# Optimization experiments

Hardware: AMD Instinct MI355X
Metric: run time of the kernel (lower is better)

## Reference

```python
import jax, jax.numpy as jnp
import numpy as np

DIM, HEADS, DIM_HEAD = 256, 8, 32  # dim == heads * dim_head
EPS = 1e-5


def setup_inputs() -> dict:
    key = jax.random.key(0)
    ks = jax.random.split(key, 6)
    B, C, H, W = 16, DIM, 64, 64
    x = jax.random.normal(ks[0], (B, C, H, W), dtype=jnp.float32)
    # 1x1 conv weights stored as [out_ch, in_ch]
    w_qkv = jax.random.normal(ks[1], (3 * DIM, DIM), dtype=jnp.float32) * (1.0 / np.sqrt(DIM))
    w_out = jax.random.normal(ks[2], (DIM, DIM), dtype=jnp.float32) * (1.0 / np.sqrt(DIM))
    b_out = jax.random.normal(ks[3], (DIM,), dtype=jnp.float32) * 0.01
    ln_gamma = jnp.ones((DIM,), dtype=jnp.float32)
    ln_beta = jnp.zeros((DIM,), dtype=jnp.float32)
    return {"x": x, "w_qkv": w_qkv, "w_out": w_out, "b_out": b_out,
            "ln_gamma": ln_gamma, "ln_beta": ln_beta}


def _linear_attention(x, w_qkv, w_out, b_out, ln_gamma, ln_beta):
    B, C, H, W = x.shape
    d = C // HEADS
    # 1x1 conv == channel matmul
    qkv = jnp.einsum('bchw,oc->bohw', x, w_qkv)  # [B, 3C, H, W]
    q, k, v = jnp.split(qkv, 3, axis=1)
    # 'b (h d) x y -> b h x y d'
    def split_heads(t):
        t = t.reshape(B, HEADS, d, H, W)
        return t.transpose(0, 1, 3, 4, 2)  # b h x y d
    q, k, v = split_heads(q), split_heads(k), split_heads(v)
    q = jax.nn.softmax(q, axis=-1)   # over d (channel) dim
    k = jax.nn.softmax(k, axis=-2)   # over y spatial axis (faithful to torch dim=-2)
    context = jnp.einsum('bhxyd,bhxye->bhde', k, v)          # [B,H,d,d]
    out = jnp.einsum('bhde,bhxye->bhxyd', context, q)        # [B,H,X,Y,d]
    # 'b h x y d -> b (h d) x y'
    out = out.transpose(0, 1, 4, 2, 3).reshape(B, C, H, W)
    # output 1x1 conv + bias
    out = jnp.einsum('bchw,oc->bohw', out, w_out) + b_out[None, :, None, None]
    # LayerNorm over channel dim (permute to NHWC, norm last axis, permute back)
    y = out.transpose(0, 2, 3, 1)  # b h w c
    mu = jnp.mean(y, axis=-1, keepdims=True)
    var = jnp.var(y, axis=-1, keepdims=True)
    y = (y - mu) / jnp.sqrt(var + EPS) * ln_gamma + ln_beta
    return y.transpose(0, 3, 1, 2)


def reference(x, w_qkv, w_out, b_out, ln_gamma, ln_beta):
    return _linear_attention(x, w_qkv, w_out, b_out, ln_gamma, ln_beta)
```

## Files before the change

kernel.cpp:

```cpp
#include <hip/hip_runtime.h>
#include <hip/hip_bf16.h>

#define NB 16
#define CDIM 256
#define NHEADS 8
#define DH 32
#define NSP 4096
#define O3 768

typedef __bf16 bf16;
typedef bf16 bf16x4 __attribute__((ext_vector_type(4)));
typedef bf16 bf16x8 __attribute__((ext_vector_type(8)));
typedef float f32x4 __attribute__((ext_vector_type(4)));
typedef float f32x16 __attribute__((ext_vector_type(16)));

static __device__ __forceinline__ float bf2f(bf16 x){ return (float)x; }
static __device__ __forceinline__ bf16 f2bf(float x){ return (bf16)x; }

static __device__ __forceinline__ void gld16(const bf16* g, bf16* l){
    __builtin_amdgcn_global_load_lds((const __attribute__((address_space(1))) void*)g,
                                     (__attribute__((address_space(3))) void*)l, 16, 0, 0);
}

__global__ void k_transpose(const float* __restrict__ x, bf16* __restrict__ xT){
    __shared__ bf16 tile[64][72];
    int b = blockIdx.z;
    int c0 = blockIdx.y * 64;
    int n0 = blockIdx.x * 64;
    int t = threadIdx.x;
    const float* xb = x + (size_t)b * CDIM * NSP;
    #pragma unroll
    for (int i = 0; i < 4; ++i){
        int lin = i*256 + t;
        int c = lin >> 4;
        int n4 = (lin & 15) * 4;
        f32x4 f = *(const f32x4*)(xb + (size_t)(c0 + c)*NSP + n0 + n4);
        bf16x4 v4;
        #pragma unroll
        for (int j = 0; j < 4; ++j) v4[j] = f2bf(f[j]);
        *(bf16x4*)&tile[c][n4] = v4;
    }
    __syncthreads();
    bf16* xTb = xT + (size_t)b * NSP * CDIM;
    #pragma unroll
    for (int i = 0; i < 2; ++i){
        int lin = i*256 + t;
        int n = lin >> 3;
        int c8 = (lin & 7) * 8;
        bf16x8 v;
        #pragma unroll
        for (int j = 0; j < 8; ++j) v[j] = tile[c8+j][n];
        *(bf16x8*)(xTb + (size_t)(n0+n)*CDIM + c0 + c8) = v;
    }
}

__global__ void k_wcvt(const float* __restrict__ w, bf16* __restrict__ w2){
    int idx = (blockIdx.x*256 + threadIdx.x) * 4;
    f32x4 f = *(const f32x4*)(w + idx);
    bf16x4 v;
    #pragma unroll
    for (int j=0;j<4;j++) v[j] = f2bf(f[j]);
    *(bf16x4*)(w2 + idx) = v;
}

__global__ __launch_bounds__(512) void k_q(const bf16* __restrict__ w2,
                                           const bf16* __restrict__ xT,
                                           bf16* __restrict__ qT){
    __shared__ union {
        bf16 Bs[32768];
        bf16 ep[64*264];
    } sm;
    int bid = blockIdx.x;
    int xcd = bid & 7, slot = bid >> 3;
    int g = xcd*64 + slot;
    int b  = g >> 5;
    int n0 = (g & 31) * 128;
    int t = threadIdx.x;
    int wv = t >> 6, lane = t & 63;

    #pragma unroll
    for (int j=0;j<8;j++){
        int base_r = wv*16 + j*2;
        int r = base_r + (lane>>5);
        int c = (lane & 31) ^ (r & 7);
        gld16(xT + ((size_t)b*NSP + n0 + r)*CDIM + c*8, &sm.Bs[(size_t)base_r*256]);
    }
    __syncthreads();

    int brow[8], brx[8];
    #pragma unroll
    for (int ni=0;ni<8;ni++){
        int r = ni*16 + (lane&15);
        brow[ni] = r*32; brx[ni] = r & 7;
    }
    int arow = wv*32 + (lane&15);
    int acol = (lane>>4)*8;

    f32x4 acc[2][8];
    #pragma unroll
    for (int i=0;i<16;i++) ((f32x4*)acc)[i] = (f32x4){0.f,0.f,0.f,0.f};

    bf16x8 af0 = *(const bf16x8*)(w2 + (size_t)(arow     )*CDIM + acol);
    bf16x8 af1 = *(const bf16x8*)(w2 + (size_t)(arow + 16)*CDIM + acol);
    #pragma unroll
    for (int k0=0;k0<8;k0++){
        bf16x8 an0, an1;
        if (k0 < 7){
            an0 = *(const bf16x8*)(w2 + (size_t)(arow     )*CDIM + (k0+1)*32 + acol);
            an1 = *(const bf16x8*)(w2 + (size_t)(arow + 16)*CDIM + (k0+1)*32 + acol);
        }
        int cbase = (lane>>4) + k0*4;
        bf16x8 bfr[8];
        #pragma unroll
        for (int ni=0;ni<8;ni++)
            bfr[ni] = *(const bf16x8*)&sm.Bs[(size_t)(brow[ni] + (cbase ^ brx[ni]))*8];
        #pragma unroll
        for (int ni=0;ni<8;ni++)
            acc[0][ni] = __builtin_amdgcn_mfma_f32_16x16x32_bf16(af0, bfr[ni], acc[0][ni], 0, 0, 0);
        #pragma unroll
        for (int ni=0;ni<8;ni++)
            acc[1][ni] = __builtin_amdgcn_mfma_f32_16x16x32_bf16(af1, bfr[ni], acc[1][ni], 0, 0, 0);
        af0 = an0; af1 = an1;
    }

    #pragma unroll
    for (int ni=0;ni<8;ni++){
        float mx = -1e30f;
        #pragma unroll
        for (int mi=0;mi<2;mi++)
            #pragma unroll
            for (int r=0;r<4;r++) mx = fmaxf(mx, acc[mi][ni][r]);
        mx = fmaxf(mx, __shfl_xor(mx, 16, 64));
        mx = fmaxf(mx, __shfl_xor(mx, 32, 64));
        float s = 0.f;
        #pragma unroll
        for (int mi=0;mi<2;mi++)
            #pragma unroll
            for (int r=0;r<4;r++){
                float e = __expf(acc[mi][ni][r] - mx);
                acc[mi][ni][r] = e; s += e;
            }
        s += __shfl_xor(s, 16, 64);
        s += __shfl_xor(s, 32, 64);
        float inv = 1.f/s;
        #pragma unroll
        for (int mi=0;mi<2;mi++)
            #pragma unroll
            for (int r=0;r<4;r++) acc[mi][ni][r] *= inv;
    }

    bf16* qTb = qT + (size_t)b * NSP * CDIM;
    #pragma unroll
    for (int ph=0; ph<2; ++ph){
        __syncthreads();
        #pragma unroll
        for (int mi=0;mi<2;mi++)
            #pragma unroll
            for (int q=0;q<4;q++){
                int ni = ph*4 + q;
                int n_loc = q*16 + (lane&15);
                int o_loc = wv*32 + mi*16 + (lane>>4)*4;
                bf16x4 v4;
                #pragma unroll
                for (int r=0;r<4;r++) v4[r] = f2bf(acc[mi][ni][r]);
                *(bf16x4*)&sm.ep[n_loc*264 + o_loc] = v4;
            }
        __syncthreads();
        #pragma unroll
        for (int i=0;i<4;i++){
            int task = i*512 + t;
            int n_loc = task >> 5, seg = task & 31;
            bf16x8 v = *(const bf16x8*)&sm.ep[n_loc*264 + seg*8];
            *(bf16x8*)(qTb + (size_t)(n0 + ph*64 + n_loc)*CDIM + seg*8) = v;
        }
    }
}

__global__ __launch_bounds__(1024,4) void k_kvctx(const bf16* __restrict__ w2,
                                                  const bf16* __restrict__ xT,
                                                  float* __restrict__ ctx_p){
    __shared__ union {
        bf16 Bs[32768];
        bf16 cb[32768];
    } sm;
    int bid = blockIdx.x;
    int xcd = bid & 7, slot = bid >> 3;
    int g = xcd*64 + slot;
    int b = g >> 5;
    int ntile = g & 31;
    int n0 = ntile * 128;
    int t = threadIdx.x;
    int wv = t >> 6, lane = t & 63;

    #pragma unroll
    for (int j=0;j<4;j++){
        int base_r = wv*8 + j*2;
        int r = base_r + (lane>>5);
        int c = (lane & 31) ^ (r & 7);
        gld16(xT + ((size_t)b*NSP + n0 + r)*CDIM + c*8, &sm.Bs[(size_t)base_r*256]);
    }
    __syncthreads();

    int brow[8], brx[8];
    #pragma unroll
    for (int ni=0;ni<8;ni++){
        int r = ni*16 + (lane&15);
        brow[ni] = r*32; brx[ni] = r & 7;
    }
    int arow = 256 + wv*32 + (lane&15);
    int acol = (lane>>4)*8;

    f32x4 acc[2][8];
    #pragma unroll
    for (int i=0;i<16;i++) ((f32x4*)acc)[i] = (f32x4){0.f,0.f,0.f,0.f};

    bf16x8 af0 = *(const bf16x8*)(w2 + (size_t)(arow     )*CDIM + acol);
    bf16x8 af1 = *(const bf16x8*)(w2 + (size_t)(arow + 16)*CDIM + acol);
    #pragma unroll
    for (int k0=0;k0<8;k0++){
        bf16x8 an0, an1;
        if (k0 < 7){
            an0 = *(const bf16x8*)(w2 + (size_t)(arow     )*CDIM + (k0+1)*32 + acol);
            an1 = *(const bf16x8*)(w2 + (size_t)(arow + 16)*CDIM + (k0+1)*32 + acol);
        }
        int cbase = (lane>>4) + k0*4;
        bf16x8 bfr[8];
        #pragma unroll
        for (int ni=0;ni<8;ni++)
            bfr[ni] = *(const bf16x8*)&sm.Bs[(size_t)(brow[ni] + (cbase ^ brx[ni]))*8];
        #pragma unroll
        for (int ni=0;ni<8;ni++)
            acc[0][ni] = __builtin_amdgcn_mfma_f32_16x16x32_bf16(af0, bfr[ni], acc[0][ni], 0, 0, 0);
        #pragma unroll
        for (int ni=0;ni<8;ni++)
            acc[1][ni] = __builtin_amdgcn_mfma_f32_16x16x32_bf16(af1, bfr[ni], acc[1][ni], 0, 0, 0);
        af0 = an0; af1 = an1;
    }

    if (wv < 8){
        #pragma unroll
        for (int mi=0;mi<2;mi++)
            #pragma unroll
            for (int r=0;r<4;r++)
                #pragma unroll
                for (int grp=0;grp<2;grp++){
                    float mx = -1e30f;
                    #pragma unroll
                    for (int q=0;q<4;q++) mx = fmaxf(mx, acc[mi][grp*4+q][r]);
                    #pragma unroll
                    for (int msk=1; msk<16; msk<<=1) mx = fmaxf(mx, __shfl_xor(mx, msk, 64));
                    float s = 0.f;
                    #pragma unroll
                    for (int q=0;q<4;q++){
                        float e = __expf(acc[mi][grp*4+q][r] - mx);
                        acc[mi][grp*4+q][r] = e; s += e;
                    }
                    #pragma unroll
                    for (int msk=1; msk<16; msk<<=1) s += __shfl_xor(s, msk, 64);
                    float inv = 1.f/s;
                    #pragma unroll
                    for (int q=0;q<4;q++) acc[mi][grp*4+q][r] *= inv;
                }
    }

    #pragma unroll
    for (int ph=0; ph<2; ++ph){
        __syncthreads();
        if (((wv>>2)&1) == ph){
            int isv  = wv >> 3;
            int w03  = wv & 3;
            int base = isv * 16384;
            #pragma unroll
            for (int mi=0;mi<2;mi++)
                #pragma unroll
                for (int ni=0;ni<8;ni++)
                    #pragma unroll
                    for (int r=0;r<4;r++){
                        int row = w03*32 + mi*16 + (lane>>4)*4 + r;
                        int n = ni*16 + (lane&15);
                        sm.cb[base + row*128 + (((n>>3) ^ (row&15))<<3) + (n&7)] = f2bf(acc[mi][ni][r]);
                    }
        }
        __syncthreads();
        if (wv < 4){
            f32x16 cacc;
            #pragma unroll
            for (int i=0;i<16;i++) cacc[i] = 0.f;
            int rr = wv*32 + (lane&31);
            #pragma unroll
            for (int s=0;s<8;s++){
                int nseg = s*2 + (lane>>5);
                int off = rr*128 + (((nseg ^ (rr&15))<<3));
                bf16x8 ka = *(const bf16x8*)&sm.cb[off];
                bf16x8 vb = *(const bf16x8*)&sm.cb[16384 + off];
                cacc = __builtin_amdgcn_mfma_f32_32x32x16_bf16(ka, vb, cacc, 0, 0, 0);
            }
            float* dst = ctx_p + ((size_t)(b*8 + ph*4 + wv)*32 + ntile)*1024;
            #pragma unroll
            for (int r=0;r<16;r++){
                int d = (r&3) + 8*(r>>2) + 4*(lane>>5);
                dst[d*32 + (lane&31)] = cacc[r];
            }
        }
    }
}

__global__ void k_merge(const float* __restrict__ w_out, const float* __restrict__ ctx_p,
                        bf16* __restrict__ W2){
    __shared__ float ctxs[32][32];
    int bh = blockIdx.x;
    int b = bh >> 3, h = bh & 7;
    int t = threadIdx.x;
    const float* base = ctx_p + (size_t)bh*32*1024;
    #pragma unroll
    for (int i=0;i<4;i++){
        int idx = i*256 + t;
        float s0 = 0.f, s1 = 0.f;
        #pragma unroll
        for (int p=0;p<16;p++){ s0 += base[(2*p)*1024 + idx]; s1 += base[(2*p+1)*1024 + idx]; }
        ((float*)ctxs)[idx] = s0 + s1;
    }
    __syncthreads();
    int o = t;
    const float* wrow = w_out + (size_t)o*CDIM + h*DH;
    float wv[32];
    #pragma unroll
    for (int d=0;d<32;d++) wv[d] = wrow[d];
    bf16* dst = W2 + ((size_t)b*CDIM + o)*CDIM + h*DH;
    #pragma unroll
    for (int g=0;g<4;g++){
        bf16x8 o8;
        #pragma unroll
        for (int jj=0;jj<8;jj++){
            int e = g*8 + jj;
            float s = 0.f;
            #pragma unroll
            for (int d=0;d<32;d++) s += wv[d]*ctxs[d][e];
            o8[jj] = f2bf(s);
        }
        *(bf16x8*)(dst + g*8) = o8;
    }
}

__global__ __launch_bounds__(256,4) void k_out_ln(const bf16* __restrict__ W2,
                                                  const bf16* __restrict__ qT,
                                                  const float* __restrict__ bout,
                                                  const float* __restrict__ gamma,
                                                  const float* __restrict__ beta,
                                                  float* __restrict__ out){
    __shared__ union {
        bf16 Bs[8192];
        float Y[256*33];
    } sm;
    __shared__ float red[2][8][32];
    __shared__ float mu_s[32], rstd_s[32];
    int bid = blockIdx.x;
    int xcd = bid & 7, slot = bid >> 3;
    int b  = slot >> 4;
    int n0 = (xcd*16 + (slot & 15)) * 32;
    int t = threadIdx.x, wv = t>>6, lane = t&63;

    const bf16* qTb = qT + (size_t)b * NSP * CDIM;
    #pragma unroll
    for (int j=0;j<4;j++){
        int base_r = wv*8 + j*2;
        int r = base_r + (lane>>5);
        int c = (lane & 31) ^ (r & 7);
        gld16(qTb + (size_t)(n0 + r)*CDIM + c*8, &sm.Bs[(size_t)base_r*256]);
    }
    __syncthreads();

    int brow[2], brx[2];
    #pragma unroll
    for (int ni=0;ni<2;ni++){
        int r = ni*16 + (lane&15);
        brow[ni] = r*32; brx[ni] = r & 7;
    }
    const bf16* Ab = W2 + (size_t)b*CDIM*CDIM;
    int arow = wv*64 + (lane&15);
    int acol = (lane>>4)*8;

    f32x4 acc[4][2];
    #pragma unroll
    for (int i=0;i<8;i++) ((f32x4*)acc)[i] = (f32x4){0.f,0.f,0.f,0.f};

    bf16x8 af[4], an[4];
    #pragma unroll
    for (int mi=0;mi<4;mi++)
        af[mi] = *(const bf16x8*)(Ab + (size_t)(arow + mi*16)*CDIM + acol);
    #pragma unroll
    for (int k0=0;k0<8;k0++){
        if (k0 < 7){
            #pragma unroll
            for (int mi=0;mi<4;mi++)
                an[mi] = *(const bf16x8*)(Ab + (size_t)(arow + mi*16)*CDIM + (k0+1)*32 + acol);
        }
        int cbase = (lane>>4) + k0*4;
        bf16x8 bfr[2];
        #pragma unroll
        for (int ni=0;ni<2;ni++)
            bfr[ni] = *(const bf16x8*)&sm.Bs[(size_t)(brow[ni] + (cbase ^ brx[ni]))*8];
        #pragma unroll
        for (int mi=0;mi<4;mi++)
            #pragma unroll
            for (int ni=0;ni<2;ni++)
                acc[mi][ni] = __builtin_amdgcn_mfma_f32_16x16x32_bf16(af[mi], bfr[ni], acc[mi][ni], 0, 0, 0);
        #pragma unroll
        for (int mi=0;mi<4;mi++) af[mi] = an[mi];
    }
    __syncthreads();
    #pragma unroll
    for (int mi=0;mi<4;mi++)
        #pragma unroll
        for (int ni=0;ni<2;ni++)
            #pragma unroll
            for (int r=0;r<4;r++){
                int o = wv*64 + mi*16 + (lane>>4)*4 + r;
                int n = ni*16 + (lane&15);
                sm.Y[o*33 + n] = acc[mi][ni][r];
            }
    __syncthreads();
    int n = t & 31, q = t >> 5;
    float s = 0.f, s2 = 0.f;
    for (int o=32*q; o<32*q+32; o++){
        float y = sm.Y[o*33+n] + bout[o];
        s += y; s2 += y*y;
    }
    red[0][q][n] = s; red[1][q][n] = s2;
    __syncthreads();
    if (t < 32){
        float S = 0.f, S2 = 0.f;
        #pragma unroll
        for (int p=0;p<8;p++){ S += red[0][p][t]; S2 += red[1][p][t]; }
        float mu = S * (1.f/256.f);
        float var = S2*(1.f/256.f) - mu*mu;
        mu_s[t] = mu; rstd_s[t] = rsqrtf(var + 1e-5f);
    }
    __syncthreads();
    float mu = mu_s[n], rstd = rstd_s[n];
    size_t ob = (size_t)b*CDIM*NSP + n0 + n;
    for (int o=32*q; o<32*q+32; o++){
        float y = sm.Y[o*33+n] + bout[o];
        out[ob + (size_t)o*NSP] = (y - mu)*rstd*gamma[o] + beta[o];
    }
}

extern "C" void kernel_launch(void* const* d_in, const int* in_sizes, int n_in,
                              void* d_out, int out_size, void* d_ws, size_t ws_size,
                              hipStream_t stream){
    const float* x     = (const float*)d_in[0];
    const float* w_qkv = (const float*)d_in[1];
    const float* w_out = (const float*)d_in[2];
    const float* b_out = (const float*)d_in[3];
    const float* gamma = (const float*)d_in[4];
    const float* beta  = (const float*)d_in[5];
    float* out = (float*)d_out;
    char* ws = (char*)d_ws;
    bf16*  xT    = (bf16*) ws;
    bf16*  qT    = (bf16*)(ws + 33554432ull);
    float* ctx_p = (float*)(ws + 67108864ull);
    bf16*  W2    = (bf16*)(ws + 134742016ull);
    bf16*  w2    = (bf16*)(ws + 136839168ull);

    k_wcvt     <<<dim3(192),       256,  0, stream>>>(w_qkv, w2);
    k_transpose<<<dim3(64, 4, NB), 256,  0, stream>>>(x, xT);
    k_kvctx    <<<dim3(512),       1024, 0, stream>>>(w2, xT, ctx_p);
    k_q        <<<dim3(512),       512,  0, stream>>>(w2, xT, qT);
    k_merge    <<<dim3(128),       256,  0, stream>>>(w_out, ctx_p, W2);
    k_out_ln   <<<dim3(2048),      256,  0, stream>>>(W2, qT, b_out, gamma, beta, out);
}
```

Before: 236.3 us.

## Fuse Q projection and softmax into the output-projection LayerNorm kernel

Removes the separate k_q kernel and computes the Q projection plus per-head channel softmax inside the output kernel. The Q tile is written back into shared memory in the swizzled layout and used directly as the B operand of the second GEMM. This avoids writing and re-reading the bf16 qT intermediate (32 MB round trip) and one launch. In exchange each block does two GEMMs, re-reads the w2 Q weights from global/L2, and holds more accumulator registers, which may reduce occupancy.

```diff
diff --git a/kernel.cpp b/kernel.cpp
--- a/kernel.cpp
+++ b/kernel.cpp
@@ -61,119 +61,6 @@
     #pragma unroll
     for (int j=0;j<4;j++) v[j] = f2bf(f[j]);
     *(bf16x4*)(w2 + idx) = v;
-}
-
-__global__ __launch_bounds__(512) void k_q(const bf16* __restrict__ w2,
-                                           const bf16* __restrict__ xT,
-                                           bf16* __restrict__ qT){
-    __shared__ union {
-        bf16 Bs[32768];
-        bf16 ep[64*264];
-    } sm;
-    int bid = blockIdx.x;
-    int xcd = bid & 7, slot = bid >> 3;
-    int g = xcd*64 + slot;
-    int b  = g >> 5;
-    int n0 = (g & 31) * 128;
-    int t = threadIdx.x;
-    int wv = t >> 6, lane = t & 63;
-
-    #pragma unroll
-    for (int j=0;j<8;j++){
-        int base_r = wv*16 + j*2;
-        int r = base_r + (lane>>5);
-        int c = (lane & 31) ^ (r & 7);
-        gld16(xT + ((size_t)b*NSP + n0 + r)*CDIM + c*8, &sm.Bs[(size_t)base_r*256]);
-    }
-    __syncthreads();
-
-    int brow[8], brx[8];
-    #pragma unroll
-    for (int ni=0;ni<8;ni++){
-        int r = ni*16 + (lane&15);
-        brow[ni] = r*32; brx[ni] = r & 7;
-    }
-    int arow = wv*32 + (lane&15);
-    int acol = (lane>>4)*8;
-
-    f32x4 acc[2][8];
-    #pragma unroll
-    for (int i=0;i<16;i++) ((f32x4*)acc)[i] = (f32x4){0.f,0.f,0.f,0.f};
-
-    bf16x8 af0 = *(const bf16x8*)(w2 + (size_t)(arow     )*CDIM + acol);
-    bf16x8 af1 = *(const bf16x8*)(w2 + (size_t)(arow + 16)*CDIM + acol);
-    #pragma unroll
-    for (int k0=0;k0<8;k0++){
-        bf16x8 an0, an1;
-        if (k0 < 7){
-            an0 = *(const bf16x8*)(w2 + (size_t)(arow     )*CDIM + (k0+1)*32 + acol);
-            an1 = *(const bf16x8*)(w2 + (size_t)(arow + 16)*CDIM + (k0+1)*32 + acol);
-        }
-        int cbase = (lane>>4) + k0*4;
-        bf16x8 bfr[8];
-        #pragma unroll
-        for (int ni=0;ni<8;ni++)
-            bfr[ni] = *(const bf16x8*)&sm.Bs[(size_t)(brow[ni] + (cbase ^ brx[ni]))*8];
-        #pragma unroll
-        for (int ni=0;ni<8;ni++)
-            acc[0][ni] = __builtin_amdgcn_mfma_f32_16x16x32_bf16(af0, bfr[ni], acc[0][ni], 0, 0, 0);
-        #pragma unroll
-        for (int ni=0;ni<8;ni++)
-            acc[1][ni] = __builtin_amdgcn_mfma_f32_16x16x32_bf16(af1, bfr[ni], acc[1][ni], 0, 0, 0);
-        af0 = an0; af1 = an1;
-    }
-
-    #pragma unroll
-    for (int ni=0;ni<8;ni++){
-        float mx = -1e30f;
-        #pragma unroll
-        for (int mi=0;mi<2;mi++)
-            #pragma unroll
-            for (int r=0;r<4;r++) mx = fmaxf(mx, acc[mi][ni][r]);
-        mx = fmaxf(mx, __shfl_xor(mx, 16, 64));
-        mx = fmaxf(mx, __shfl_xor(mx, 32, 64));
-        float s = 0.f;
-        #pragma unroll
-        for (int mi=0;mi<2;mi++)
-            #pragma unroll
-            for (int r=0;r<4;r++){
-                float e = __expf(acc[mi][ni][r] - mx);
-                acc[mi][ni][r] = e; s += e;
-            }
-        s += __shfl_xor(s, 16, 64);
-        s += __shfl_xor(s, 32, 64);
-        float inv = 1.f/s;
-        #pragma unroll
-        for (int mi=0;mi<2;mi++)
-            #pragma unroll
-            for (int r=0;r<4;r++) acc[mi][ni][r] *= inv;
-    }
-
-    bf16* qTb = qT + (size_t)b * NSP * CDIM;
-    #pragma unroll
-    for (int ph=0; ph<2; ++ph){
-        __syncthreads();
-        #pragma unroll
-        for (int mi=0;mi<2;mi++)
-            #pragma unroll
-            for (int q=0;q<4;q++){
-                int ni = ph*4 + q;
-                int n_loc = q*16 + (lane&15);
-                int o_loc = wv*32 + mi*16 + (lane>>4)*4;
-                bf16x4 v4;
-                #pragma unroll
-                for (int r=0;r<4;r++) v4[r] = f2bf(acc[mi][ni][r]);
-                *(bf16x4*)&sm.ep[n_loc*264 + o_loc] = v4;
-            }
-        __syncthreads();
-        #pragma unroll
-        for (int i=0;i<4;i++){
-            int task = i*512 + t;
-            int n_loc = task >> 5, seg = task & 31;
-            bf16x8 v = *(const bf16x8*)&sm.ep[n_loc*264 + seg*8];
-            *(bf16x8*)(qTb + (size_t)(n0 + ph*64 + n_loc)*CDIM + seg*8) = v;
-        }
-    }
 }
 
 __global__ __launch_bounds__(1024,4) void k_kvctx(const bf16* __restrict__ w2,
@@ -342,12 +229,13 @@
     }
 }
 
-__global__ __launch_bounds__(256,4) void k_out_ln(const bf16* __restrict__ W2,
-                                                  const bf16* __restrict__ qT,
-                                                  const float* __restrict__ bout,
-                                                  const float* __restrict__ gamma,
-                                                  const float* __restrict__ beta,
-                                                  float* __restrict__ out){
+__global__ __launch_bounds__(256,4) void k_qout_ln(const bf16* __restrict__ w2,
+                                                   const bf16* __restrict__ xT,
+                                                   const bf16* __restrict__ W2,
+                                                   const float* __restrict__ bout,
+                                                   const float* __restrict__ gamma,
+                                                   const float* __restrict__ beta,
+                                                   float* __restrict__ out){
     __shared__ union {
         bf16 Bs[8192];
         float Y[256*33];
@@ -360,13 +248,13 @@
     int n0 = (xcd*16 + (slot & 15)) * 32;
     int t = threadIdx.x, wv = t>>6, lane = t&63;
 
-    const bf16* qTb = qT + (size_t)b * NSP * CDIM;
+    const bf16* xTb = xT + (size_t)b * NSP * CDIM;
     #pragma unroll
     for (int j=0;j<4;j++){
         int base_r = wv*8 + j*2;
         int r = base_r + (lane>>5);
         int c = (lane & 31) ^ (r & 7);
-        gld16(qTb + (size_t)(n0 + r)*CDIM + c*8, &sm.Bs[(size_t)base_r*256]);
+        gld16(xTb + (size_t)(n0 + r)*CDIM + c*8, &sm.Bs[(size_t)base_r*256]);
     }
     __syncthreads();
 
@@ -376,38 +264,112 @@
         int r = ni*16 + (lane&15);
         brow[ni] = r*32; brx[ni] = r & 7;
     }
-    const bf16* Ab = W2 + (size_t)b*CDIM*CDIM;
     int arow = wv*64 + (lane&15);
     int acol = (lane>>4)*8;
 
     f32x4 acc[4][2];
     #pragma unroll
     for (int i=0;i<8;i++) ((f32x4*)acc)[i] = (f32x4){0.f,0.f,0.f,0.f};
-
-    bf16x8 af[4], an[4];
+    {
+        bf16x8 af[4], an[4];
+        #pragma unroll
+        for (int mi=0;mi<4;mi++)
+            af[mi] = *(const bf16x8*)(w2 + (size_t)(arow + mi*16)*CDIM + acol);
+        #pragma unroll
+        for (int k0=0;k0<8;k0++){
+            if (k0 < 7){
+                #pragma unroll
+                for (int mi=0;mi<4;mi++)
+                    an[mi] = *(const bf16x8*)(w2 + (size_t)(arow + mi*16)*CDIM + (k0+1)*32 + acol);
+            }
+            int cbase = (lane>>4) + k0*4;
+            bf16x8 bfr[2];
+            #pragma unroll
+            for (int ni=0;ni<2;ni++)
+                bfr[ni] = *(const bf16x8*)&sm.Bs[(size_t)(brow[ni] + (cbase ^ brx[ni]))*8];
+            #pragma unroll
+            for (int mi=0;mi<4;mi++)
+                #pragma unroll
+                for (int ni=0;ni<2;ni++)
+                    acc[mi][ni] = __builtin_amdgcn_mfma_f32_16x16x32_bf16(af[mi], bfr[ni], acc[mi][ni], 0, 0, 0);
+            #pragma unroll
+            for (int mi=0;mi<4;mi++) af[mi] = an[mi];
+        }
+    }
+
+    #pragma unroll
+    for (int ni=0;ni<2;ni++)
+        #pragma unroll
+        for (int hp=0;hp<2;hp++){
+            float mx = -1e30f;
+            #pragma unroll
+            for (int mi=2*hp; mi<2*hp+2; mi++)
+                #pragma unroll
+                for (int r=0;r<4;r++) mx = fmaxf(mx, acc[mi][ni][r]);
+            mx = fmaxf(mx, __shfl_xor(mx, 16, 64));
+            mx = fmaxf(mx, __shfl_xor(mx, 32, 64));
+            float s = 0.f;
+            #pragma unroll
+            for (int mi=2*hp; mi<2*hp+2; mi++)
+                #pragma unroll
+                for (int r=0;r<4;r++){
+                    float e = __expf(acc[mi][ni][r] - mx);
+                    acc[mi][ni][r] = e; s += e;
+                }
+            s += __shfl_xor(s, 16, 64);
+            s += __shfl_xor(s, 32, 64);
+            float inv = 1.f/s;
+            #pragma unroll
+            for (int mi=2*hp; mi<2*hp+2; mi++)
+                #pragma unroll
+                for (int r=0;r<4;r++) acc[mi][ni][r] *= inv;
+        }
+
+    __syncthreads();
     #pragma unroll
     for (int mi=0;mi<4;mi++)
-        af[mi] = *(const bf16x8*)(Ab + (size_t)(arow + mi*16)*CDIM + acol);
-    #pragma unroll
-    for (int k0=0;k0<8;k0++){
-        if (k0 < 7){
+        #pragma unroll
+        for (int ni=0;ni<2;ni++){
+            int n_loc = ni*16 + (lane&15);
+            int cseg  = wv*8 + mi*2 + (lane>>5);
+            bf16x4 v4;
+            #pragma unroll
+            for (int r=0;r<4;r++) v4[r] = f2bf(acc[mi][ni][r]);
+            *(bf16x4*)&sm.Bs[(size_t)(n_loc*32 + (cseg ^ (n_loc&7)))*8 + ((lane>>4)&1)*4] = v4;
+        }
+    __syncthreads();
+
+    const bf16* Ab = W2 + (size_t)b*CDIM*CDIM;
+    f32x4 acc2[4][2];
+    #pragma unroll
+    for (int i=0;i<8;i++) ((f32x4*)acc2)[i] = (f32x4){0.f,0.f,0.f,0.f};
+    {
+        bf16x8 af[4], an[4];
+        #pragma unroll
+        for (int mi=0;mi<4;mi++)
+            af[mi] = *(const bf16x8*)(Ab + (size_t)(arow + mi*16)*CDIM + acol);
+        #pragma unroll
+        for (int k0=0;k0<8;k0++){
+            if (k0 < 7){
+                #pragma unroll
+                for (int mi=0;mi<4;mi++)
+                    an[mi] = *(const bf16x8*)(Ab + (size_t)(arow + mi*16)*CDIM + (k0+1)*32 + acol);
+            }
+            int cbase = (lane>>4) + k0*4;
+            bf16x8 bfr[2];
+            #pragma unroll
+            for (int ni=0;ni<2;ni++)
+                bfr[ni] = *(const bf16x8*)&sm.Bs[(size_t)(brow[ni] + (cbase ^ brx[ni]))*8];
             #pragma unroll
             for (int mi=0;mi<4;mi++)
-                an[mi] = *(const bf16x8*)(Ab + (size_t)(arow + mi*16)*CDIM + (k0+1)*32 + acol);
-        }
-        int cbase = (lane>>4) + k0*4;
-        bf16x8 bfr[2];
-        #pragma unroll
-        for (int ni=0;ni<2;ni++)
-            bfr[ni] = *(const bf16x8*)&sm.Bs[(size_t)(brow[ni] + (cbase ^ brx[ni]))*8];
-        #pragma unroll
-        for (int mi=0;mi<4;mi++)
-            #pragma unroll
-            for (int ni=0;ni<2;ni++)
-                acc[mi][ni] = __builtin_amdgcn_mfma_f32_16x16x32_bf16(af[mi], bfr[ni], acc[mi][ni], 0, 0, 0);
-        #pragma unroll
-        for (int mi=0;mi<4;mi++) af[mi] = an[mi];
-    }
+                #pragma unroll
+                for (int ni=0;ni<2;ni++)
+                    acc2[mi][ni] = __builtin_amdgcn_mfma_f32_16x16x32_bf16(af[mi], bfr[ni], acc2[mi][ni], 0, 0, 0);
+            #pragma unroll
+            for (int mi=0;mi<4;mi++) af[mi] = an[mi];
+        }
+    }
+
     __syncthreads();
     #pragma unroll
     for (int mi=0;mi<4;mi++)
@@ -417,7 +379,7 @@
             for (int r=0;r<4;r++){
                 int o = wv*64 + mi*16 + (lane>>4)*4 + r;
                 int n = ni*16 + (lane&15);
-                sm.Y[o*33 + n] = acc[mi][ni][r];
+                sm.Y[o*33 + n] = acc2[mi][ni][r];
             }
     __syncthreads();
     int n = t & 31, q = t >> 5;
@@ -457,7 +419,6 @@
     float* out = (float*)d_out;
     char* ws = (char*)d_ws;
     bf16*  xT    = (bf16*) ws;
-    bf16*  qT    = (bf16*)(ws + 33554432ull);
     float* ctx_p = (float*)(ws + 67108864ull);
     bf16*  W2    = (bf16*)(ws + 134742016ull);
     bf16*  w2    = (bf16*)(ws + 136839168ull);
@@ -465,7 +426,6 @@
     k_wcvt     <<<dim3(192),       256,  0, stream>>>(w_qkv, w2);
     k_transpose<<<dim3(64, 4, NB), 256,  0, stream>>>(x, xT);
     k_kvctx    <<<dim3(512),       1024, 0, stream>>>(w2, xT, ctx_p);
-    k_q        <<<dim3(512),       512,  0, stream>>>(w2, xT, qT);
     k_merge    <<<dim3(128),       256,  0, stream>>>(w_out, ctx_p, W2);
-    k_out_ln   <<<dim3(2048),      256,  0, stream>>>(W2, qT, b_out, gamma, beta, out);
-}
+    k_qout_ln  <<<dim3(2048),      256,  0, stream>>>(w2, xT, W2, b_out, gamma, beta, out);
+}
```

Result: no change. 237.9 us (+0.7%).
